# Performance work log

Measured on AMD Instinct MI355X. Metric: run time of the kernel, lower is better.

## Reference

```python
import jax, jax.numpy as jnp
import numpy as np

EMBED_DIM = 512
POS_DIM = 192
NUM_HEADS = 8
QUERY_HEAD_DIM = 32
POS_HEAD_DIM = 4
SEQ_LEN = 1024
BATCH = 8
IN_PROJ_DIM = (QUERY_HEAD_DIM * 2 + POS_HEAD_DIM) * NUM_HEADS  # 544


def setup_inputs() -> dict:
    key = jax.random.key(0)
    ks = jax.random.split(key, 5)
    x = jax.random.normal(ks[0], (SEQ_LEN, BATCH, EMBED_DIM), dtype=jnp.float32)
    pos_emb = jax.random.normal(ks[1], (1, 2 * SEQ_LEN - 1, POS_DIM), dtype=jnp.float32)
    key_padding_mask = jnp.zeros((BATCH, SEQ_LEN), dtype=bool)
    # ScaledLinear(embed_dim, in_proj_dim) with initial_scale=query_head_dim**-0.25
    in_proj_w = jax.random.normal(ks[2], (IN_PROJ_DIM, EMBED_DIM), dtype=jnp.float32) * (EMBED_DIM ** -0.5) * (QUERY_HEAD_DIM ** -0.25)
    in_proj_b = jax.random.normal(ks[3], (IN_PROJ_DIM,), dtype=jnp.float32) * 0.01
    # ScaledLinear(pos_dim, num_heads*pos_head_dim, bias=False, initial_scale=0.05)
    linear_pos_w = jax.random.normal(ks[4], (NUM_HEADS * POS_HEAD_DIM, POS_DIM), dtype=jnp.float32) * (POS_DIM ** -0.5) * 0.05
    return {"x": x, "pos_emb": pos_emb, "key_padding_mask": key_padding_mask,
            "in_proj_w": in_proj_w, "in_proj_b": in_proj_b, "linear_pos_w": linear_pos_w}


def reference(x, pos_emb, key_padding_mask, in_proj_w, in_proj_b, linear_pos_w):
    S, B, _ = x.shape
    H, QD, PD = NUM_HEADS, QUERY_HEAD_DIM, POS_HEAD_DIM
    proj = jnp.einsum('sbe,oe->sbo', x, in_proj_w) + in_proj_b  # (S,B,544)
    qdim = H * QD
    q = proj[..., :qdim].reshape(S, B, H, QD).transpose(2, 1, 0, 3)          # (H,B,S,QD)
    k = proj[..., qdim:2 * qdim].reshape(S, B, H, QD).transpose(2, 1, 3, 0)  # (H,B,QD,S)
    p = proj[..., 2 * qdim:].reshape(S, B, H, PD).transpose(2, 1, 0, 3)      # (H,B,S,PD)
    attn_scores = jnp.matmul(q, k)  # (H,B,S,S)
    # positional scores
    pe = jnp.einsum('ltd,od->lto', pos_emb, linear_pos_w)                    # (1,2S-1,H*PD)
    pe = pe.reshape(1, 2 * S - 1, H, PD).transpose(2, 0, 3, 1)               # (H,1,PD,2S-1)
    pos_scores = jnp.matmul(p, pe)                                           # (H,B,S,2S-1)
    # rel-shift: out[h,b,i,j] = pos_scores[h,b,i, (S-1) + j - i]
    idx = (S - 1) + jnp.arange(S)[None, :] - jnp.arange(S)[:, None]          # (S,S)
    pos_scores = jnp.take_along_axis(pos_scores, idx[None, None], axis=-1)   # (H,B,S,S)
    attn_scores = attn_scores + pos_scores
    attn_scores = jnp.where(key_padding_mask[None, :, None, :], -jnp.inf, attn_scores)
    return jax.nn.softmax(attn_scores, axis=-1)
```

## Files before the change

### kernel.cpp

```cpp
#include <hip/hip_runtime.h>
#include <math.h>

#define S_LEN 1024
#define BATCH 8
#define NH 8
#define QD 32
#define PD 4
#define EMB 512
#define NPROJ 544
#define LPOS 2047

typedef __attribute__((ext_vector_type(8))) short short8;
typedef __attribute__((ext_vector_type(4))) float f32x4;
typedef __attribute__((ext_vector_type(4))) unsigned int u32x4;
typedef __attribute__((ext_vector_type(2))) unsigned int u32x2;

union U4 { u32x4 u; short8 s; };

static __device__ inline unsigned short f2bf(float f) {
    unsigned int u = __builtin_bit_cast(unsigned int, f);
    u += 0x7fffu + ((u >> 16) & 1u);
    return (unsigned short)(u >> 16);
}

#define NXV 1048576
#define NWV 69632
__global__ __launch_bounds__(256) void convert_kernel(
    const float* __restrict__ X, const float* __restrict__ W,
    unsigned short* __restrict__ Xb, unsigned short* __restrict__ Wb)
{
    int idx = blockIdx.x * 256 + threadIdx.x;
    const f32x4* src;
    unsigned short* dst;
    int i;
    if (idx < NXV)            { src = (const f32x4*)X; dst = Xb; i = idx; }
    else if (idx < NXV + NWV) { src = (const f32x4*)W; dst = Wb; i = idx - NXV; }
    else return;
    f32x4 v = src[i];
    union { unsigned short s[4]; u32x2 u; } pk;
    pk.s[0] = f2bf(v.x); pk.s[1] = f2bf(v.y);
    pk.s[2] = f2bf(v.z); pk.s[3] = f2bf(v.w);
    ((u32x2*)dst)[i] = pk.u;
}

__global__ __launch_bounds__(256) void proj_kernel(
    const unsigned short* __restrict__ Xb, const unsigned short* __restrict__ Wb,
    const float* __restrict__ bias,
    unsigned short* __restrict__ Qb, unsigned short* __restrict__ Kb,
    unsigned short* __restrict__ Pb)
{
    const int tid = threadIdx.x;
    const int wv = tid >> 6, lane = tid & 63;
    const int n16 = lane & 15, quad = lane >> 4;
    const int m0 = blockIdx.x * 64, o0 = blockIdx.y * 64;
    const int m = m0 + wv * 16 + n16;

    f32x4 acc[4] = {{0,0,0,0},{0,0,0,0},{0,0,0,0},{0,0,0,0}};
    const unsigned short* xrow = Xb + (size_t)m * EMB;

#pragma unroll 4
    for (int k0 = 0; k0 < EMB; k0 += 32) {
        U4 bx; bx.u = *(const u32x4*)(xrow + k0 + quad * 8);
#pragma unroll
        for (int ot = 0; ot < 4; ++ot) {
            int o = o0 + ot * 16 + n16;
            int oc = o < NPROJ ? o : NPROJ - 1;
            U4 aw; aw.u = *(const u32x4*)(Wb + (size_t)oc * EMB + k0 + quad * 8);
            acc[ot] = __builtin_amdgcn_mfma_f32_16x16x32_bf16(aw.s, bx.s, acc[ot], 0, 0, 0);
        }
    }

    const int s = m >> 3, b = m & 7;
#pragma unroll
    for (int ot = 0; ot < 4; ++ot) {
        int obase = o0 + ot * 16 + quad * 4;
        if (obase >= NPROJ) continue;
        f32x4 bv = *(const f32x4*)(bias + obase);
        union { unsigned short sh[4]; u32x2 u; } pk;
        pk.sh[0] = f2bf(acc[ot].x + bv.x);
        pk.sh[1] = f2bf(acc[ot].y + bv.y);
        pk.sh[2] = f2bf(acc[ot].z + bv.z);
        pk.sh[3] = f2bf(acc[ot].w + bv.w);
        unsigned short* dst;
        if (obase < 256) {
            int h = obase >> 5, d = obase & 31;
            dst = Qb + (((size_t)(h * BATCH + b)) * S_LEN + s) * QD + d;
        } else if (obase < 512) {
            int o2 = obase - 256;
            int h = o2 >> 5, d = o2 & 31;
            dst = Kb + (((size_t)(h * BATCH + b)) * S_LEN + s) * QD + d;
        } else {
            int h = (obase - 512) >> 2;
            dst = Pb + (((size_t)(h * BATCH + b)) * S_LEN + s) * PD;
        }
        *(u32x2*)dst = pk.u;
    }
}

__global__ __launch_bounds__(256) void pe_kernel(
    const float* __restrict__ pos, const float* __restrict__ Wp,
    unsigned short* __restrict__ PEr)
{
    int o = blockIdx.x * 256 + threadIdx.x;
    if (o >= LPOS * 32) return;
    int l = o >> 5, ht = o & 31;
    const f32x4* pr = (const f32x4*)(pos + (size_t)l * 192);
    const f32x4* wr = (const f32x4*)(Wp + (size_t)ht * 192);
    float acc = 0.0f;
#pragma unroll 8
    for (int d = 0; d < 48; ++d) {
        f32x4 a = pr[d], w = wr[d];
        acc += a.x * w.x + a.y * w.y + a.z * w.z + a.w * w.w;
    }
    int h = ht >> 2, t = ht & 3, w = 2046 - l;
    PEr[((size_t)h * LPOS + w) * PD + t] = f2bf(acc);
}

__global__ __launch_bounds__(256) void attn_kernel(
    const unsigned short* __restrict__ Qb, const unsigned short* __restrict__ Kb,
    const unsigned short* __restrict__ Pb, const u32x2* __restrict__ PEr,
    const unsigned char* __restrict__ mask, float* __restrict__ out)
{
    __shared__ u32x2 pe_w[1040];
    __shared__ float madd[S_LEN];
    __shared__ float redm[4][16];
    __shared__ float reds[4][16];

    const int hb = blockIdx.y;
    const int h = hb >> 3, b = hb & 7;
    const int i0 = blockIdx.x * 16;
    const int tid = threadIdx.x;
    const int wv = tid >> 6, lane = tid & 63;
    const int n16 = lane & 15, quad = lane >> 4;

    const u32x2* src = PEr + (size_t)h * LPOS + i0;
    for (int wl = tid; wl < 1039; wl += 256) pe_w[wl] = src[wl];
    for (int j = tid; j < S_LEN; j += 256)
        madd[j] = mask[b * S_LEN + j] ? -INFINITY : 0.0f;

    U4 b1; b1.u = *(const u32x4*)(Qb + ((size_t)hb * S_LEN + i0 + n16) * QD + quad * 8);
    u32x2 p4 = *(const u32x2*)(Pb + ((size_t)hb * S_LEN + i0 + n16) * PD);
    U4 b2, b3;
    b2.u.x = (n16 == 2 * quad)     ? p4.x : 0u;
    b2.u.y = (n16 == 2 * quad)     ? p4.y : 0u;
    b2.u.z = (n16 == 2 * quad + 1) ? p4.x : 0u;
    b2.u.w = (n16 == 2 * quad + 1) ? p4.y : 0u;
    b3.u.x = (n16 == 2 * quad + 8) ? p4.x : 0u;
    b3.u.y = (n16 == 2 * quad + 8) ? p4.y : 0u;
    b3.u.z = (n16 == 2 * quad + 9) ? p4.x : 0u;
    b3.u.w = (n16 == 2 * quad + 9) ? p4.y : 0u;

    __syncthreads();

    f32x4 sc[16];
    const unsigned short* kbase = Kb + (size_t)hb * S_LEN * QD;

#pragma unroll
    for (int t = 0; t < 16; ++t) {
        const int j0 = wv * 256 + t * 16;
        U4 a1; a1.u = *(const u32x4*)(kbase + (j0 + n16) * QD + quad * 8);
        const int w = 1023 - j0 - n16 + 2 * quad;
        u32x2 e0 = pe_w[w], e1 = pe_w[w + 1];
        u32x2 e8 = pe_w[w + 8], e9 = pe_w[w + 9];
        U4 a2; a2.u.x = e0.x; a2.u.y = e0.y; a2.u.z = e1.x; a2.u.w = e1.y;
        U4 a3; a3.u.x = e8.x; a3.u.y = e8.y; a3.u.z = e9.x; a3.u.w = e9.y;
        f32x4 acc = {0.0f, 0.0f, 0.0f, 0.0f};
        acc = __builtin_amdgcn_mfma_f32_16x16x32_bf16(a3.s, b3.s, acc, 0, 0, 0);
        acc = __builtin_amdgcn_mfma_f32_16x16x32_bf16(a2.s, b2.s, acc, 0, 0, 0);
        acc = __builtin_amdgcn_mfma_f32_16x16x32_bf16(a1.s, b1.s, acc, 0, 0, 0);
        f32x4 mv = *(const f32x4*)&madd[j0 + quad * 4];
        sc[t] = acc + mv;
    }

    float mx = -INFINITY;
#pragma unroll
    for (int t = 0; t < 16; ++t) {
        mx = fmaxf(mx, fmaxf(fmaxf(sc[t].x, sc[t].y), fmaxf(sc[t].z, sc[t].w)));
    }
    mx = fmaxf(mx, __shfl_xor(mx, 16));
    mx = fmaxf(mx, __shfl_xor(mx, 32));
    if (quad == 0) redm[wv][n16] = mx;
    __syncthreads();
    mx = fmaxf(fmaxf(redm[0][n16], redm[1][n16]),
               fmaxf(redm[2][n16], redm[3][n16]));

    float sum = 0.0f;
#pragma unroll
    for (int t = 0; t < 16; ++t) {
        sc[t].x = __expf(sc[t].x - mx);
        sc[t].y = __expf(sc[t].y - mx);
        sc[t].z = __expf(sc[t].z - mx);
        sc[t].w = __expf(sc[t].w - mx);
        sum += sc[t].x + sc[t].y + sc[t].z + sc[t].w;
    }
    sum += __shfl_xor(sum, 16);
    sum += __shfl_xor(sum, 32);
    if (quad == 0) reds[wv][n16] = sum;
    __syncthreads();
    const float tot = reds[0][n16] + reds[1][n16] + reds[2][n16] + reds[3][n16];
    const float inv = 1.0f / tot;

    float* orow = out + ((size_t)hb * S_LEN + i0 + n16) * S_LEN;
#pragma unroll
    for (int t = 0; t < 16; ++t) {
        const int j0 = wv * 256 + t * 16 + quad * 4;
        f32x4 o4 = sc[t] * inv;
        *(f32x4*)(orow + j0) = o4;
    }
}

extern "C" void kernel_launch(void* const* d_in, const int* in_sizes, int n_in,
                              void* d_out, int out_size, void* d_ws, size_t ws_size,
                              hipStream_t stream) {
    (void)in_sizes; (void)n_in; (void)out_size; (void)ws_size;
    const float* x           = (const float*)d_in[0];
    const float* pos_emb     = (const float*)d_in[1];
    const unsigned char* msk = (const unsigned char*)d_in[2];
    const float* in_proj_w   = (const float*)d_in[3];
    const float* in_proj_b   = (const float*)d_in[4];
    const float* linear_posw = (const float*)d_in[5];
    float* out = (float*)d_out;

    char* p = (char*)d_ws;
    unsigned short* Qb  = (unsigned short*)p; p += (size_t)4 << 20;
    unsigned short* Kb  = (unsigned short*)p; p += (size_t)4 << 20;
    unsigned short* Pb  = (unsigned short*)p; p += 524288;
    unsigned short* PEr = (unsigned short*)p; p += 131072;
    unsigned short* Xb  = (unsigned short*)p; p += (size_t)8 << 20;
    unsigned short* Wb  = (unsigned short*)p; p += 557056;

    convert_kernel<<<4368, 256, 0, stream>>>(x, in_proj_w, Xb, Wb);
    pe_kernel<<<256, 256, 0, stream>>>(pos_emb, linear_posw, PEr);
    proj_kernel<<<dim3(128, 9), 256, 0, stream>>>(Xb, Wb, in_proj_b, Qb, Kb, Pb);
    attn_kernel<<<dim3(64, 64), 256, 0, stream>>>(Qb, Kb, Pb, (const u32x2*)PEr, msk, out);
}
```

Baseline: 361.1 us.

## Stage weights in LDS, pair positional rows, use nontemporal stores

The projection kernel now stages 64 weight rows per block in padded shared memory in two K phases, instead of each wave reloading them from global memory. The attention kernel pre-packs adjacent positional-embedding entries into 16-byte pairs in LDS, so each MFMA operand is a single vector load instead of four 8-byte loads. It also adds an occupancy hint to launch bounds and writes the large softmax output with nontemporal stores to avoid polluting the cache. The pair table doubles LDS use in attention, and the weight staging adds barriers to the projection.

```diff
diff --git a/kernel.cpp b/kernel.cpp
--- a/kernel.cpp
+++ b/kernel.cpp
@@ -43,30 +43,45 @@
     ((u32x2*)dst)[i] = pk.u;
 }
 
+#define WROW 264
 __global__ __launch_bounds__(256) void proj_kernel(
     const unsigned short* __restrict__ Xb, const unsigned short* __restrict__ Wb,
     const float* __restrict__ bias,
     unsigned short* __restrict__ Qb, unsigned short* __restrict__ Kb,
     unsigned short* __restrict__ Pb)
 {
+    __shared__ unsigned short wlds[64 * WROW];
+
     const int tid = threadIdx.x;
     const int wv = tid >> 6, lane = tid & 63;
     const int n16 = lane & 15, quad = lane >> 4;
     const int m0 = blockIdx.x * 64, o0 = blockIdx.y * 64;
     const int m = m0 + wv * 16 + n16;
+    const unsigned short* xrow = Xb + (size_t)m * EMB;
 
     f32x4 acc[4] = {{0,0,0,0},{0,0,0,0},{0,0,0,0},{0,0,0,0}};
-    const unsigned short* xrow = Xb + (size_t)m * EMB;
-
-#pragma unroll 4
-    for (int k0 = 0; k0 < EMB; k0 += 32) {
-        U4 bx; bx.u = *(const u32x4*)(xrow + k0 + quad * 8);
-#pragma unroll
-        for (int ot = 0; ot < 4; ++ot) {
-            int o = o0 + ot * 16 + n16;
-            int oc = o < NPROJ ? o : NPROJ - 1;
-            U4 aw; aw.u = *(const u32x4*)(Wb + (size_t)oc * EMB + k0 + quad * 8);
-            acc[ot] = __builtin_amdgcn_mfma_f32_16x16x32_bf16(aw.s, bx.s, acc[ot], 0, 0, 0);
+
+#pragma unroll
+    for (int phase = 0; phase < 2; ++phase) {
+        __syncthreads();
+#pragma unroll
+        for (int u = 0; u < 8; ++u) {
+            int idx = tid + 256 * u;
+            int r = idx >> 5, c = idx & 31;
+            int o = o0 + r; if (o > NPROJ - 1) o = NPROJ - 1;
+            u32x4 v = *(const u32x4*)(Wb + (size_t)o * EMB + phase * 256 + c * 8);
+            *(u32x4*)(wlds + r * WROW + c * 8) = v;
+        }
+        __syncthreads();
+#pragma unroll
+        for (int kk = 0; kk < 8; ++kk) {
+            const int k0 = kk * 32;
+            U4 bx; bx.u = *(const u32x4*)(xrow + phase * 256 + k0 + quad * 8);
+#pragma unroll
+            for (int ot = 0; ot < 4; ++ot) {
+                U4 aw; aw.u = *(const u32x4*)(wlds + (ot * 16 + n16) * WROW + k0 + quad * 8);
+                acc[ot] = __builtin_amdgcn_mfma_f32_16x16x32_bf16(aw.s, bx.s, acc[ot], 0, 0, 0);
+            }
         }
     }
 
@@ -116,12 +131,12 @@
     PEr[((size_t)h * LPOS + w) * PD + t] = f2bf(acc);
 }
 
-__global__ __launch_bounds__(256) void attn_kernel(
+__global__ __launch_bounds__(256, 3) void attn_kernel(
     const unsigned short* __restrict__ Qb, const unsigned short* __restrict__ Kb,
     const unsigned short* __restrict__ Pb, const u32x2* __restrict__ PEr,
     const unsigned char* __restrict__ mask, float* __restrict__ out)
 {
-    __shared__ u32x2 pe_w[1040];
+    __shared__ u32x4 pe_pair[1040];
     __shared__ float madd[S_LEN];
     __shared__ float redm[4][16];
     __shared__ float reds[4][16];
@@ -134,7 +149,12 @@
     const int n16 = lane & 15, quad = lane >> 4;
 
     const u32x2* src = PEr + (size_t)h * LPOS + i0;
-    for (int wl = tid; wl < 1039; wl += 256) pe_w[wl] = src[wl];
+    for (int wl = tid; wl < 1039; wl += 256) {
+        u32x2 lo = src[wl];
+        u32x2 hi = (i0 + wl + 1 <= LPOS - 1) ? src[wl + 1] : lo;
+        u32x4 v; v.x = lo.x; v.y = lo.y; v.z = hi.x; v.w = hi.y;
+        pe_pair[wl] = v;
+    }
     for (int j = tid; j < S_LEN; j += 256)
         madd[j] = mask[b * S_LEN + j] ? -INFINITY : 0.0f;
 
@@ -153,30 +173,26 @@
     __syncthreads();
 
     f32x4 sc[16];
-    const unsigned short* kbase = Kb + (size_t)hb * S_LEN * QD;
+    const unsigned short* kbase =
+        Kb + (size_t)hb * S_LEN * QD + (size_t)(wv * 256 + n16) * QD + quad * 8;
+    const int wbase = 1023 - wv * 256 - n16 + 2 * quad;
 
 #pragma unroll
     for (int t = 0; t < 16; ++t) {
-        const int j0 = wv * 256 + t * 16;
-        U4 a1; a1.u = *(const u32x4*)(kbase + (j0 + n16) * QD + quad * 8);
-        const int w = 1023 - j0 - n16 + 2 * quad;
-        u32x2 e0 = pe_w[w], e1 = pe_w[w + 1];
-        u32x2 e8 = pe_w[w + 8], e9 = pe_w[w + 9];
-        U4 a2; a2.u.x = e0.x; a2.u.y = e0.y; a2.u.z = e1.x; a2.u.w = e1.y;
-        U4 a3; a3.u.x = e8.x; a3.u.y = e8.y; a3.u.z = e9.x; a3.u.w = e9.y;
+        U4 a1; a1.u = *(const u32x4*)(kbase + t * 16 * QD);
+        U4 a2; a2.u = pe_pair[wbase - t * 16];
+        U4 a3; a3.u = pe_pair[wbase - t * 16 + 8];
         f32x4 acc = {0.0f, 0.0f, 0.0f, 0.0f};
         acc = __builtin_amdgcn_mfma_f32_16x16x32_bf16(a3.s, b3.s, acc, 0, 0, 0);
         acc = __builtin_amdgcn_mfma_f32_16x16x32_bf16(a2.s, b2.s, acc, 0, 0, 0);
         acc = __builtin_amdgcn_mfma_f32_16x16x32_bf16(a1.s, b1.s, acc, 0, 0, 0);
-        f32x4 mv = *(const f32x4*)&madd[j0 + quad * 4];
-        sc[t] = acc + mv;
+        sc[t] = acc + *(const f32x4*)&madd[wv * 256 + t * 16 + quad * 4];
     }
 
     float mx = -INFINITY;
 #pragma unroll
-    for (int t = 0; t < 16; ++t) {
+    for (int t = 0; t < 16; ++t)
         mx = fmaxf(mx, fmaxf(fmaxf(sc[t].x, sc[t].y), fmaxf(sc[t].z, sc[t].w)));
-    }
     mx = fmaxf(mx, __shfl_xor(mx, 16));
     mx = fmaxf(mx, __shfl_xor(mx, 32));
     if (quad == 0) redm[wv][n16] = mx;
@@ -205,7 +221,7 @@
     for (int t = 0; t < 16; ++t) {
         const int j0 = wv * 256 + t * 16 + quad * 4;
         f32x4 o4 = sc[t] * inv;
-        *(f32x4*)(orow + j0) = o4;
+        __builtin_nontemporal_store(o4, (f32x4*)(orow + j0));
     }
 }
 
```

Result: faster. 352.4 us (-2.4%).
